# Performance work log

Hardware: AMD Instinct MI355X
Metric: run time of the kernel (lower is better)

## Reference

```python
import jax, jax.numpy as jnp
import numpy as np

D_MODEL = 1024
H = 4
DK = 128   # head_qk_dim (key_dim=512)
DV = 256   # head_v_dim (value_dim=1024)
EPS = 1e-5
SCALE = DK ** -0.5


def setup_inputs() -> dict:
    key = jax.random.key(0)
    ks = jax.random.split(key, 8)
    w = lambda k, i, o: jax.random.normal(k, (i, o), jnp.float32) * (2.0 ** -2.5) * (6.0 / (i + o)) ** 0.5 * 2
    return {
        "x": jax.random.normal(ks[0], (2, 4096, D_MODEL), jnp.float32),
        "Wq": w(ks[1], D_MODEL, H * DK),
        "Wk": w(ks[2], D_MODEL, H * DK),
        "Wv": w(ks[3], D_MODEL, H * DV),
        "Wb": w(ks[4], D_MODEL, H),
        "Wg": w(ks[5], D_MODEL, H * DV),
        "Wo": w(ks[6], H * DV, D_MODEL),
        "norm_w": jnp.ones((DV,), jnp.float32),
    }


def _delta_rule(q, k, v, beta):
    """Delta-rule linear attention. q,k: [b,n,h,dk], v: [b,n,h,dv], beta: [b,n,h].
    S_t = S_{t-1} + k_t (beta_t * (v_t - k_t^T S_{t-1}))^T ; o_t = q_t^T S_t."""
    b = q.shape[0]
    # time-major for scan: [n,b,h,*]
    qt = jnp.moveaxis(q, 1, 0)
    kt = jnp.moveaxis(k, 1, 0)
    vt = jnp.moveaxis(v, 1, 0)
    bt = jnp.moveaxis(beta, 1, 0)
    S0 = jnp.zeros((b, H, DK, DV), q.dtype)

    def step(S, inp):
        q_t, k_t, v_t, b_t = inp
        pred = jnp.einsum('bhk,bhkv->bhv', k_t, S)          # current memory readout
        delta = (v_t - pred) * b_t[..., None]                # beta-scaled error
        S = S + k_t[..., :, None] * delta[..., None, :]      # rank-1 update [b,h,dk,dv]
        o_t = jnp.einsum('bhk,bhkv->bhv', q_t, S)
        return S, o_t

    _, o = jax.lax.scan(step, S0, (qt, kt, vt, bt))          # o: [n,b,h,dv]
    return jnp.moveaxis(o, 0, 1)                             # [b,n,h,dv]


def reference(x, Wq, Wk, Wv, Wb, Wg, Wo, norm_w):
    b, n, _ = x.shape
    q = (x @ Wq).reshape(b, n, H, DK)
    k = (x @ Wk).reshape(b, n, H, DK)
    v = (x @ Wv).reshape(b, n, H, DV)
    beta = jax.nn.sigmoid(x @ Wb)                            # [b,n,h]
    # L2-normalize keys (delta-rule kernels assume unit-norm k) and scale q
    k = k * jax.lax.rsqrt(jnp.sum(k * k, axis=-1, keepdims=True) + 1e-12)
    q = q * SCALE
    o = _delta_rule(q, k, v, beta)                           # [b,n,h,dv]
    # FusedRMSNormSwishGate over head_v_dim
    g = (x @ Wg).reshape(b, n, H, DV)
    o = o * jax.lax.rsqrt(jnp.mean(o * o, axis=-1, keepdims=True) + EPS) * norm_w
    o = o * (g * jax.nn.sigmoid(g))                          # swish gate
    return o.reshape(b, n, H * DV) @ Wo
```

## Files before the change

### kernel.cpp

```cpp
#include <hip/hip_runtime.h>
#include <hip/hip_bf16.h>
#include <stdint.h>
#include <stddef.h>

typedef __attribute__((ext_vector_type(8))) short short8v;
typedef __attribute__((ext_vector_type(4))) float f32x4;
typedef unsigned short us;

__device__ __forceinline__ float bf2f(unsigned short u) {
    return __uint_as_float(((unsigned int)u) << 16);
}
__device__ __forceinline__ unsigned short f2bf(float f) {
    unsigned int x = __float_as_uint(f);
    x += 0x7fffu + ((x >> 16) & 1u);
    return (unsigned short)(x >> 16);
}
__device__ __forceinline__ unsigned int cvtpk(float lo, float hi) {
    unsigned int r;
    asm("v_cvt_pk_bf16_f32 %0, %1, %2" : "=v"(r) : "v"(lo), "v"(hi));
    return r;
}

#define NTOK 8192
#define DM   1024
#define NPROJ 3072
#define SEQ  4096
#define NCHUNK 64
#define SCQ 0.08838834764831845f

#define GLDS16(g, l) __builtin_amdgcn_global_load_lds( \
    (const __attribute__((address_space(1))) void*)(g), \
    (__attribute__((address_space(3))) void*)(l), 16, 0, 0)

__device__ __forceinline__ void bar_lgkm() {
    asm volatile("s_waitcnt lgkmcnt(0)" ::: "memory");
    __builtin_amdgcn_s_barrier();
    __builtin_amdgcn_sched_barrier(0);
}

__device__ __forceinline__ int sw16(int row, int k) {
    int u = k >> 3;
    int us_ = (u & 8) | ((u ^ row) & 7);
    return row * 128 + us_ * 8 + (k & 7);
}
__device__ __forceinline__ int sw8(int row, int k) {
    int u = k >> 3;
    int us_ = (u ^ row) & 7;
    return row * 64 + us_ * 8 + (k & 7);
}
__device__ __forceinline__ int sw128(int row, int k) {
    int u = k >> 3;
    return row * 128 + ((u ^ row) & 15) * 8 + (k & 7);
}
__device__ __forceinline__ int sw64(int row, int k) {
    int u = k >> 3;
    return row * 64 + ((u ^ row) & 7) * 8 + (k & 7);
}
__device__ __forceinline__ int sw64b(int row, int k) {
    int u = k >> 3;
    return row * 64 + ((u ^ row ^ (row >> 3)) & 7) * 8 + (k & 7);
}
__device__ __forceinline__ int swU(int t, int j) {
    int jj = j & 127, u = jj >> 3;
    int us_ = (u & 8) | ((u ^ t) & 7);
    return t * 256 + (j >> 7) * 128 + us_ * 8 + (jj & 7);
}
__device__ __forceinline__ int swU128(int t, int jj) {
    int u = jj >> 3;
    int us_ = (u & 8) | ((u ^ t) & 7);
    return t * 128 + us_ * 8 + (jj & 7);
}

__global__ void convert_x(const float* __restrict__ x, us* __restrict__ xb, int nunits) {
    int i = blockIdx.x * 256 + threadIdx.x;
    if (i >= nunits) return;
    int tok = i >> 7;
    int kb = (i >> 3) & 15;
    int u = i & 7;
    int ko = kb * 64 + ((u ^ (tok & 7)) * 8);
    const float4* src = (const float4*)(x + (size_t)tok * 1024 + ko);
    float4 v0 = src[0], v1 = src[1];
    uint4 o;
    o.x = cvtpk(v0.x, v0.y); o.y = cvtpk(v0.z, v0.w);
    o.z = cvtpk(v1.x, v1.y); o.w = cvtpk(v1.z, v1.w);
    *(uint4*)(xb + (size_t)i * 8) = o;
}

__global__ __launch_bounds__(256) void transpose_w(const float* __restrict__ src,
                                                   us* __restrict__ dst, int K, int N) {
    __shared__ float tl[64][65];
    int k0 = blockIdx.y * 64, n0 = blockIdx.x * 64;
    int tid = threadIdx.x;
    int tr = tid >> 6, tc = tid & 63;
    #pragma unroll
    for (int i = 0; i < 16; i++) {
        int kk = 4 * i + tr;
        tl[kk][tc] = src[(size_t)(k0 + kk) * N + n0 + tc];
    }
    __syncthreads();
    int n = tid >> 2, seg = (tid & 3) * 16;
    short8v a, b;
    #pragma unroll
    for (int e = 0; e < 8; e++) {
        a[e] = (short)f2bf(tl[seg + e][n]);
        b[e] = (short)f2bf(tl[seg + 8 + e][n]);
    }
    int n_ = n0 + n;
    int o1 = (tid & 3) * 2, o2_ = o1 + 1;
    us* d = dst + (size_t)n_ * K + k0;
    *(short8v*)(d + (o1 ^ (n_ & 7)) * 8) = a;
    *(short8v*)(d + (o2_ ^ (n_ & 7)) * 8) = b;
}

__global__ __launch_bounds__(256) void beta_kernel(const float* __restrict__ x,
                                                   const float* __restrict__ Wb,
                                                   float* __restrict__ beta) {
    __shared__ float part[16][16][4];
    int tl = threadIdx.x >> 4, sg = threadIdx.x & 15;
    int tok = blockIdx.x * 16 + tl;
    const float4* xr = (const float4*)(x + (size_t)tok * DM);
    const float4* wb = (const float4*)Wb;
    float s0 = 0.f, s1 = 0.f, s2 = 0.f, s3 = 0.f;
    #pragma unroll
    for (int it = 0; it < 16; it++) {
        int f = it * 16 + sg;
        float4 xv = xr[f];
        float4 w0 = wb[4 * f + 0], w1 = wb[4 * f + 1], w2 = wb[4 * f + 2], w3 = wb[4 * f + 3];
        s0 += xv.x * w0.x + xv.y * w1.x + xv.z * w2.x + xv.w * w3.x;
        s1 += xv.x * w0.y + xv.y * w1.y + xv.z * w2.y + xv.w * w3.y;
        s2 += xv.x * w0.z + xv.y * w1.z + xv.z * w2.z + xv.w * w3.z;
        s3 += xv.x * w0.w + xv.y * w1.w + xv.z * w2.w + xv.w * w3.w;
    }
    part[tl][sg][0] = s0; part[tl][sg][1] = s1; part[tl][sg][2] = s2; part[tl][sg][3] = s3;
    __syncthreads();
    if (threadIdx.x < 64) {
        int tl2 = threadIdx.x >> 2, h = threadIdx.x & 3;
        float s = 0.f;
        #pragma unroll
        for (int g = 0; g < 16; g++) s += part[tl2][g][h];
        beta[(size_t)(blockIdx.x * 16 + tl2) * 4 + h] = 1.f / (1.f + __expf(-s));
    }
}

template<int OUT_F32>
__global__ __launch_bounds__(256) void gemm_bt(
    const us* __restrict__ A, const us* __restrict__ BT,
    void* __restrict__ C, int M, int N, int K)
{
    __shared__ us As[128][64];
    __shared__ us Bs[128][64];
    int tid = threadIdx.x;
    int wave = tid >> 6, lane = tid & 63;
    int wr = (wave >> 1) * 64, wc = (wave & 1) * 64;
    int fr = lane & 15, fq = lane >> 4;
    int nbx = gridDim.x, nwg = nbx * gridDim.y;
    int wg = blockIdx.y * nbx + blockIdx.x;
    int cpx = nwg >> 3;
    wg = (wg & 7) * cpx + (wg >> 3);
    int m0 = (wg % nbx) * 128, n0 = (wg / nbx) * 128;

    f32x4 acc[4][4];
    #pragma unroll
    for (int i = 0; i < 4; i++)
        #pragma unroll
        for (int j = 0; j < 4; j++) acc[i][j] = (f32x4){0.f, 0.f, 0.f, 0.f};

    int rl = lane >> 3, ul = lane & 7;

    for (int k0 = 0; k0 < K; k0 += 64) {
        #pragma unroll
        for (int i = 0; i < 4; i++) {
            int row = wave * 32 + i * 8 + rl;
            GLDS16(&A[(size_t)(m0 + row) * K + k0 + ul * 8], &As[0][0] + (wave * 32 + i * 8) * 64);
            GLDS16(&BT[(size_t)(n0 + row) * K + k0 + ul * 8], &Bs[0][0] + (wave * 32 + i * 8) * 64);
        }
        __syncthreads();
        #pragma unroll
        for (int kk = 0; kk < 2; kk++) {
            short8v a[4], b[4];
            #pragma unroll
            for (int i = 0; i < 4; i++) {
                int ra = wr + i * 16 + fr;
                a[i] = *(const short8v*)&As[ra][((4 * kk + fq) ^ (ra & 7)) * 8];
                int rb = wc + i * 16 + fr;
                b[i] = *(const short8v*)&Bs[rb][((4 * kk + fq) ^ (rb & 7)) * 8];
            }
            #pragma unroll
            for (int i = 0; i < 4; i++)
                #pragma unroll
                for (int j = 0; j < 4; j++)
                    acc[i][j] = __builtin_amdgcn_mfma_f32_16x16x32_bf16(a[i], b[j], acc[i][j], 0, 0, 0);
        }
        __syncthreads();
    }
    #pragma unroll
    for (int i = 0; i < 4; i++)
        #pragma unroll
        for (int j = 0; j < 4; j++)
            #pragma unroll
            for (int t = 0; t < 4; t++) {
                int row = m0 + wr + i * 16 + fq * 4 + t;
                int col = n0 + wc + j * 16 + fr;
                float val = acc[i][j][t];
                if (OUT_F32) ((float*)C)[(size_t)row * N + col] = val;
                else ((us*)C)[(size_t)row * N + col] = f2bf(val);
            }
}

__global__ __launch_bounds__(256) void chunk_pre(
    const us* __restrict__ QKVG, const float* __restrict__ beta,
    us* __restrict__ Wbuf, us* __restrict__ Ubuf,
    us* __restrict__ Pbuf, us* __restrict__ KTbuf)
{
    __shared__ us Ks[8192];
    __shared__ us KTs[8192];
    __shared__ us VT[8192];
    __shared__ us Tb[4096];
    __shared__ float Af[64][64];
    __shared__ float betas[64];

    int c = blockIdx.x, bh = blockIdx.y;
    int b = bh >> 2, h = bh & 3;
    int tid = threadIdx.x;
    int wv = tid >> 6, ln = tid & 63;
    int fr = ln & 15, fq = ln >> 4;
    int tok0 = b * SEQ + c * 64;
    size_t cb = (size_t)bh * NCHUNK + c;

    #pragma unroll
    for (int r = 0; r < 4; r++) {
        int idx = tid + 256 * r;
        int t = idx >> 4, u = idx & 15;
        short8v kv = *(const short8v*)(QKVG + (size_t)(tok0 + t) * NPROJ + 512 + h * 128 + u * 8);
        *(short8v*)(Ks + sw16(t, u * 8)) = kv;
    }
    if (tid < 64) betas[tid] = beta[(size_t)(tok0 + tid) * 4 + h];
    __syncthreads();

    {
        int t = tid >> 2, p = tid & 3;
        short8v v[4];
        float ss = 0.f;
        #pragma unroll
        for (int uu = 0; uu < 4; uu++) {
            v[uu] = *(const short8v*)(Ks + sw16(t, (p * 4 + uu) * 8));
            #pragma unroll
            for (int e = 0; e < 8; e++) {
                float f = bf2f((unsigned short)v[uu][e]);
                ss += f * f;
            }
        }
        ss += __shfl_xor(ss, 1);
        ss += __shfl_xor(ss, 2);
        float rn = rsqrtf(ss + 1e-12f);
        #pragma unroll
        for (int uu = 0; uu < 4; uu++) {
            short8v o;
            #pragma unroll
            for (int e = 0; e < 8; e++)
                o[e] = (short)f2bf(bf2f((unsigned short)v[uu][e]) * rn);
            *(short8v*)(Ks + sw16(t, (p * 4 + uu) * 8)) = o;
        }
    }
    __syncthreads();

    {
        f32x4 aacc[4];
        #pragma unroll
        for (int jt = 0; jt < 4; jt++) aacc[jt] = (f32x4){0.f, 0.f, 0.f, 0.f};
        #pragma unroll
        for (int ks = 0; ks < 4; ks++) {
            short8v ak = *(const short8v*)(Ks + sw16(16 * wv + fr, 32 * ks + 8 * fq));
            #pragma unroll
            for (int jt = 0; jt < 4; jt++) {
                short8v bk = *(const short8v*)(Ks + sw16(16 * jt + fr, 32 * ks + 8 * fq));
                aacc[jt] = __builtin_amdgcn_mfma_f32_16x16x32_bf16(ak, bk, aacc[jt], 0, 0, 0);
            }
        }
        #pragma unroll
        for (int jt = 0; jt < 4; jt++)
            #pragma unroll
            for (int r = 0; r < 4; r++) {
                int t = 16 * wv + 4 * fq + r, s = 16 * jt + fr;
                if (s < t) Af[t][s] = betas[t] * aacc[jt][r];
            }
    }
    __syncthreads();

    if (wv == 0) {
        int cc = ln;
        for (int tb = 0; tb < 8; tb++) {
            int base = tb * 8;
            float xs[8];
            #pragma unroll
            for (int i = 0; i < 8; i++) {
                int t = base + i;
                float v = Af[t][cc];
                #pragma unroll
                for (int s = 0; s < i; s++)
                    v += Af[t][base + s] * xs[s];
                float xt = (cc < t) ? -v : 0.f;
                xs[i] = xt;
                if (cc < t) Af[t][cc] = xt;
            }
            for (int r = base + 8; r < 64; r += 2) {
                float u0 = 0.f, u1 = 0.f;
                #pragma unroll
                for (int s = 0; s < 8; s++) {
                    float a0 = Af[r][base + s];
                    float a1 = Af[r + 1][base + s];
                    u0 += a0 * xs[s];
                    u1 += a1 * xs[s];
                }
                Af[r][cc] += u0;
                Af[r + 1][cc] += u1;
            }
        }
    } else {
        int q = tid - 64;
        for (int g = q; g < 1024; g += 192) {
            int t = g >> 4, u = g & 15;
            short8v kv = *(const short8v*)(Ks + sw16(t, u * 8));
            #pragma unroll
            for (int e = 0; e < 8; e++)
                KTs[sw64b(u * 8 + e, t)] = (unsigned short)kv[e];
        }
        for (int g = q; g < 1024; g += 192) {
            int t = g >> 4, jg = g & 15;
            short8v vv = *(const short8v*)(QKVG + (size_t)(tok0 + t) * NPROJ + 1024 + h * 256 + jg * 8);
            #pragma unroll
            for (int e = 0; e < 8; e++)
                VT[sw64b(jg * 8 + e, t)] = (unsigned short)vv[e];
        }
    }
    __syncthreads();

    {
        f32x4 pacc[4];
        #pragma unroll
        for (int jt = 0; jt < 4; jt++) pacc[jt] = (f32x4){0.f, 0.f, 0.f, 0.f};
        #pragma unroll
        for (int ks = 0; ks < 4; ks++) {
            short8v aq = *(const short8v*)(QKVG + (size_t)(tok0 + 16 * wv + fr) * NPROJ + h * 128 + ks * 32 + fq * 8);
            #pragma unroll
            for (int jt = 0; jt < 4; jt++) {
                short8v bk = *(const short8v*)(Ks + sw16(16 * jt + fr, 32 * ks + 8 * fq));
                pacc[jt] = __builtin_amdgcn_mfma_f32_16x16x32_bf16(aq, bk, pacc[jt], 0, 0, 0);
            }
        }
        #pragma unroll
        for (int jt = 0; jt < 4; jt++)
            #pragma unroll
            for (int r = 0; r < 4; r++) {
                int t = 16 * wv + 4 * fq + r, s = 16 * jt + fr;
                float val = (s <= t) ? pacc[jt][r] * SCQ : 0.f;
                Pbuf[cb * 4096 + sw64(t, s)] = f2bf(val);
            }
        #pragma unroll
        for (int i = 0; i < 16; i++) {
            int idx = tid + 256 * i;
            int t = idx >> 6, s = idx & 63;
            float tv = (s < t) ? Af[t][s] : (s == t ? 1.f : 0.f);
            Tb[sw8(t, s)] = f2bf(tv * betas[s]);
        }
        #pragma unroll
        for (int i = 0; i < 4; i++) {
            int idx = tid + 256 * i;
            *(short8v*)(KTbuf + cb * 8192 + (size_t)idx * 8) =
                *(const short8v*)(KTs + (size_t)idx * 8);
        }
    }
    __syncthreads();

    {
        f32x4 wacc[8], uacc[8];
        #pragma unroll
        for (int jt = 0; jt < 8; jt++) {
            wacc[jt] = (f32x4){0.f, 0.f, 0.f, 0.f};
            uacc[jt] = (f32x4){0.f, 0.f, 0.f, 0.f};
        }
        #pragma unroll
        for (int ks = 0; ks < 2; ks++) {
            short8v at = *(const short8v*)(Tb + sw8(16 * wv + fr, 32 * ks + 8 * fq));
            #pragma unroll
            for (int jt = 0; jt < 8; jt++) {
                short8v bk = *(const short8v*)(KTs + sw64b(16 * jt + fr, 32 * ks + 8 * fq));
                wacc[jt] = __builtin_amdgcn_mfma_f32_16x16x32_bf16(at, bk, wacc[jt], 0, 0, 0);
                short8v bv = *(const short8v*)(VT + sw64b(16 * jt + fr, 32 * ks + 8 * fq));
                uacc[jt] = __builtin_amdgcn_mfma_f32_16x16x32_bf16(at, bv, uacc[jt], 0, 0, 0);
            }
        }
        #pragma unroll
        for (int jt = 0; jt < 8; jt++)
            #pragma unroll
            for (int r = 0; r < 4; r++) {
                int t = 16 * wv + 4 * fq + r, d = 16 * jt + fr;
                Wbuf[cb * 8192 + (d >> 6) * 4096 + sw64(t, d & 63)] = f2bf(-wacc[jt][r]);
                Ubuf[cb * 16384 + swU(t, d)] = f2bf(uacc[jt][r]);
            }
    }
    __syncthreads();

    #pragma unroll
    for (int i = 0; i < 4; i++) {
        int g = tid + 256 * i;
        int t = g >> 4, jg = g & 15;
        short8v vv = *(const short8v*)(QKVG + (size_t)(tok0 + t) * NPROJ + 1024 + h * 256 + 128 + jg * 8);
        #pragma unroll
        for (int e = 0; e < 8; e++)
            VT[sw64b(jg * 8 + e, t)] = (unsigned short)vv[e];
    }
    __syncthreads();
    {
        f32x4 uacc[8];
        #pragma unroll
        for (int jt = 0; jt < 8; jt++) uacc[jt] = (f32x4){0.f, 0.f, 0.f, 0.f};
        #pragma unroll
        for (int ks = 0; ks < 2; ks++) {
            short8v at = *(const short8v*)(Tb + sw8(16 * wv + fr, 32 * ks + 8 * fq));
            #pragma unroll
            for (int jt = 0; jt < 8; jt++) {
                short8v bv = *(const short8v*)(VT + sw64b(16 * jt + fr, 32 * ks + 8 * fq));
                uacc[jt] = __builtin_amdgcn_mfma_f32_16x16x32_bf16(at, bv, uacc[jt], 0, 0, 0);
            }
        }
        #pragma unroll
        for (int jt = 0; jt < 8; jt++)
            #pragma unroll
            for (int r = 0; r < 4; r++) {
                int t = 16 * wv + 4 * fq + r, j = 16 * jt + fr;
                Ubuf[cb * 16384 + swU(t, 128 + j)] = f2bf(uacc[jt][r]);
            }
    }
}

#define SCW 0
#define SCKT 8192
#define SCU 16384
#define SCBUF 17408
#define SSTB (2 * SCBUF)
#define SDTB (2 * SCBUF + 2048)

__global__ __launch_bounds__(128, 1) void scan_mfma(
    const us* __restrict__ Wbuf, const us* __restrict__ Ubuf,
    const us* __restrict__ KTbuf, us* __restrict__ Sbuf)
{
    extern __shared__ us lds[];
    int tid = threadIdx.x;
    int wv = tid >> 6, ln = tid & 63;
    int fr = ln & 15, fq = ln >> 4;
    int sl = blockIdx.x >> 3;
    int j0 = sl * 16;
    int bh = blockIdx.x & 7;

    short8v id0;
    #pragma unroll
    for (int e = 0; e < 8; e++)
        id0[e] = (short)((8 * fq + e == fr) ? 0x3F80 : 0);

    f32x4 sacc[4];
    #pragma unroll
    for (int i = 0; i < 4; i++) sacc[i] = (f32x4){0.f, 0.f, 0.f, 0.f};

    us* ST = lds + SSTB + wv * 1024;

    auto issue = [&](int c1) {
        size_t cb = (size_t)bh * NCHUNK + c1;
        us* dst = lds + (c1 & 1) * SCBUF;
        const us* Wc = Wbuf + cb * 8192 + wv * 4096;
        const us* Kc = KTbuf + cb * 8192 + wv * 4096;
        #pragma unroll
        for (int i = 0; i < 8; i++) {
            GLDS16(Wc + i * 512 + ln * 8, dst + SCW + wv * 4096 + i * 512);
            GLDS16(Kc + i * 512 + ln * 8, dst + SCKT + wv * 4096 + i * 512);
        }
        if (wv) {
            const us* Uc = Ubuf + cb * 16384;
            #pragma unroll
            for (int i = 0; i < 2; i++) {
                int t = i * 32 + (ln >> 1);
                GLDS16(Uc + swU(t, j0 + (ln & 1) * 8), dst + SCU + i * 512);
            }
        }
    };

    issue(0);

    for (int c = 0; c < NCHUNK; c++) {
        const us* ba = lds + (c & 1) * SCBUF;
        us* DTw = lds + SDTB + (c & 1) * 2048 + wv * 1024;
        const us* DTr = lds + SDTB + (c & 1) * 2048;
        size_t sb = ((size_t)bh * NCHUNK + c) * 32768 + sl * 2048 + wv * 1024;

        #pragma unroll
        for (int dt = 0; dt < 4; dt++) {
            uint2 w;
            w.x = cvtpk(sacc[dt][0], sacc[dt][1]);
            w.y = cvtpk(sacc[dt][2], sacc[dt][3]);
            int dl = 16 * dt + 4 * fq;
            int off = fr * 64 + (((dl >> 3) ^ fr) & 7) * 8 + (dl & 7);
            *(uint2*)&ST[off] = w;
            *(uint2*)(Sbuf + sb + off) = w;
        }
        if (c + 1 < NCHUNK) issue(c + 1);
        if (c + 1 < NCHUNK) {
            if (wv) asm volatile("s_waitcnt vmcnt(22)" ::: "memory");
            else    asm volatile("s_waitcnt vmcnt(20)" ::: "memory");
        } else {
            asm volatile("s_waitcnt vmcnt(4)" ::: "memory");
        }
        __builtin_amdgcn_sched_barrier(0);

        f32x4 dacc[4];
        #pragma unroll
        for (int tt = 0; tt < 4; tt++) dacc[tt] = (f32x4){0.f, 0.f, 0.f, 0.f};
        #pragma unroll
        for (int kc = 0; kc < 2; kc++) {
            short8v bs = *(const short8v*)&ST[fr * 64 + (((4 * kc + fq) ^ fr) & 7) * 8];
            #pragma unroll
            for (int tt = 0; tt < 4; tt++) {
                short8v aw = *(const short8v*)&ba[SCW + wv * 4096 + sw64(16 * tt + fr, 32 * kc + 8 * fq)];
                dacc[tt] = __builtin_amdgcn_mfma_f32_16x16x32_bf16(aw, bs, dacc[tt], 0, 0, 0);
            }
        }
        if (wv) {
            #pragma unroll
            for (int tt = 0; tt < 4; tt++) {
                short8v au = *(const short8v*)&ba[SCU + (16 * tt + fr) * 16 + 8 * (fq & 1)];
                dacc[tt] = __builtin_amdgcn_mfma_f32_16x16x32_bf16(au, id0, dacc[tt], 0, 0, 0);
            }
        }
        #pragma unroll
        for (int tt = 0; tt < 4; tt++) {
            uint2 w;
            w.x = cvtpk(dacc[tt][0], dacc[tt][1]);
            w.y = cvtpk(dacc[tt][2], dacc[tt][3]);
            int tl = 16 * tt + 4 * fq;
            *(uint2*)&DTw[fr * 64 + (((tl >> 3) ^ fr) & 7) * 8 + (tl & 7)] = w;
        }
        bar_lgkm();
        #pragma unroll
        for (int kc2 = 0; kc2 < 2; kc2++) {
            int o = fr * 64 + (((4 * kc2 + fq) ^ fr) & 7) * 8;
            short8v bd0 = *(const short8v*)&DTr[o];
            short8v bd1 = *(const short8v*)&DTr[1024 + o];
            #pragma unroll
            for (int dt = 0; dt < 4; dt++) {
                short8v ak = *(const short8v*)&ba[SCKT + sw64b(64 * wv + 16 * dt + fr, 32 * kc2 + 8 * fq)];
                sacc[dt] = __builtin_amdgcn_mfma_f32_16x16x32_bf16(ak, bd0, sacc[dt], 0, 0, 0);
                sacc[dt] = __builtin_amdgcn_mfma_f32_16x16x32_bf16(ak, bd1, sacc[dt], 0, 0, 0);
            }
        }
    }
}

#define K2_W 0
#define K2_P 8192
#define K2_U 12288
#define K2_S 20480
#define K2_Q 36864
#define K2_DT 45056

__global__ __launch_bounds__(256, 1) void out_k(
    const us* __restrict__ QKVG, const us* __restrict__ Wbuf,
    const us* __restrict__ Ubuf, const us* __restrict__ Pbuf,
    const us* __restrict__ Sbuf, us* __restrict__ Ob)
{
    extern __shared__ us lds[];
    int tid = threadIdx.x;
    int wv = tid >> 6, ln = tid & 63;
    int fr = ln & 15, fq = ln >> 4;
    int c = blockIdx.x;
    int bh = blockIdx.y >> 1, jh = blockIdx.y & 1;
    int b = bh >> 2, h = bh & 3;
    int tok0 = b * SEQ + c * 64;
    size_t cb = (size_t)bh * NCHUNK + c;

    short8v id0, id1;
    #pragma unroll
    for (int e = 0; e < 8; e++) {
        id0[e] = (short)((8 * fq + e == fr) ? 0x3F80 : 0);
        id1[e] = (short)((8 * fq + e == fr + 16) ? 0x3F80 : 0);
    }

    #pragma unroll
    for (int i = 0; i < 4; i++) {
        int q = (i * 4 + wv) * 512 + ln * 8;
        GLDS16(Wbuf + cb * 8192 + q, lds + K2_W + (i * 4 + wv) * 512);
    }
    #pragma unroll
    for (int i = 0; i < 2; i++) {
        int q = (i * 4 + wv) * 512 + ln * 8;
        GLDS16(Pbuf + cb * 4096 + q, lds + K2_P + (i * 4 + wv) * 512);
    }
    #pragma unroll
    for (int i = 0; i < 4; i++) {
        int q = (i * 4 + wv) * 512 + ln * 8;
        int t = q >> 7, r = q & 127;
        GLDS16(Ubuf + cb * 16384 + t * 256 + jh * 128 + r, lds + K2_U + (i * 4 + wv) * 512);
    }
    size_t sbase = cb * 32768 + (size_t)jh * 16384;
    #pragma unroll
    for (int i = 0; i < 8; i++) {
        int q = (i * 4 + wv) * 512 + ln * 8;
        GLDS16(Sbuf + sbase + q, lds + K2_S + (i * 4 + wv) * 512);
    }
    short8v qv[4];
    #pragma unroll
    for (int i = 0; i < 4; i++) {
        int idx = tid + 256 * i;
        int t = idx >> 4, u = idx & 15;
        qv[i] = *(const short8v*)(QKVG + (size_t)(tok0 + t) * NPROJ + h * 128 + u * 8);
    }
    #pragma unroll
    for (int i = 0; i < 4; i++) {
        int idx = tid + 256 * i;
        int t = idx >> 4, u = idx & 15;
        *(short8v*)&lds[K2_Q + sw128(t, u * 8)] = qv[i];
    }
    __syncthreads();

    f32x4 dacc[8], oacc[8];
    #pragma unroll
    for (int jt = 0; jt < 8; jt++) {
        dacc[jt] = (f32x4){0.f, 0.f, 0.f, 0.f};
        oacc[jt] = (f32x4){0.f, 0.f, 0.f, 0.f};
    }
    #pragma unroll
    for (int ks = 0; ks < 4; ks++) {
        short8v aw = *(const short8v*)&lds[K2_W + (ks >> 1) * 4096
            + sw64(16 * wv + fr, (ks & 1) * 32 + 8 * fq)];
        short8v aq = *(const short8v*)&lds[K2_Q + sw128(16 * wv + fr, 32 * ks + 8 * fq)];
        #pragma unroll
        for (int jt = 0; jt < 8; jt++) {
            short8v bs = *(const short8v*)&lds[K2_S + jt * 2048 + (ks >> 1) * 1024
                + fr * 64 + ((((ks & 1) * 4 + fq) ^ fr) & 7) * 8];
            dacc[jt] = __builtin_amdgcn_mfma_f32_16x16x32_bf16(aw, bs, dacc[jt], 0, 0, 0);
            oacc[jt] = __builtin_amdgcn_mfma_f32_16x16x32_bf16(aq, bs, oacc[jt], 0, 0, 0);
        }
    }
    #pragma unroll
    for (int ju = 0; ju < 4; ju++) {
        short8v au = *(const short8v*)&lds[K2_U + swU128(16 * wv + fr, 32 * ju + 8 * fq)];
        dacc[2 * ju + 0] = __builtin_amdgcn_mfma_f32_16x16x32_bf16(au, id0, dacc[2 * ju + 0], 0, 0, 0);
        dacc[2 * ju + 1] = __builtin_amdgcn_mfma_f32_16x16x32_bf16(au, id1, dacc[2 * ju + 1], 0, 0, 0);
    }
    #pragma unroll
    for (int jt = 0; jt < 8; jt++)
        #pragma unroll
        for (int r = 0; r < 4; r++) oacc[jt][r] *= SCQ;
    #pragma unroll
    for (int jt = 0; jt < 8; jt++) {
        int j = 16 * jt + fr;
        int t0 = 16 * wv + 4 * fq;
        uint2 w;
        w.x = cvtpk(dacc[jt][0], dacc[jt][1]);
        w.y = cvtpk(dacc[jt][2], dacc[jt][3]);
        *(uint2*)&lds[K2_DT + sw64(j, t0)] = w;
    }
    bar_lgkm();

    #pragma unroll
    for (int ks = 0; ks < 2; ks++) {
        short8v ap = *(const short8v*)&lds[K2_P + sw64(16 * wv + fr, 32 * ks + 8 * fq)];
        #pragma unroll
        for (int jt = 0; jt < 8; jt++) {
            short8v bd = *(const short8v*)&lds[K2_DT + sw64(16 * jt + fr, 32 * ks + 8 * fq)];
            oacc[jt] = __builtin_amdgcn_mfma_f32_16x16x32_bf16(ap, bd, oacc[jt], 0, 0, 0);
        }
    }
    us* ob = Ob + (size_t)tok0 * 1024 + h * 256 + jh * 128;
    #pragma unroll
    for (int jt = 0; jt < 8; jt++)
        #pragma unroll
        for (int r = 0; r < 4; r++) {
            int t = 16 * wv + 4 * fq + r;
            ob[(size_t)t * 1024 + 16 * jt + fr] = f2bf(oacc[jt][r]);
        }
}

__global__ __launch_bounds__(256) void gate_norm(const us* __restrict__ Ob,
                                                 const us* __restrict__ QKVG,
                                                 const float* __restrict__ norm_w,
                                                 us* __restrict__ o2)
{
    int gid = blockIdx.x * 4 + (threadIdx.x >> 6);
    int ln = threadIdx.x & 63;
    int tok = gid >> 2, h = gid & 3;
    size_t base = (size_t)tok * 1024 + h * 256 + ln * 4;
    uint2 ov = *(const uint2*)&Ob[base];
    float o0 = bf2f((us)ov.x), o1 = bf2f((us)(ov.x >> 16));
    float o2v = bf2f((us)ov.y), o3 = bf2f((us)(ov.y >> 16));
    float ss = o0 * o0 + o1 * o1 + o2v * o2v + o3 * o3;
    #pragma unroll
    for (int off = 32; off; off >>= 1) ss += __shfl_xor(ss, off);
    float r = rsqrtf(ss * (1.0f / 256.0f) + 1e-5f);
    uint2 gv = *(const uint2*)&QKVG[(size_t)tok * NPROJ + 2048 + h * 256 + ln * 4];
    float g0 = bf2f((us)gv.x), g1 = bf2f((us)(gv.x >> 16));
    float g2 = bf2f((us)gv.y), g3 = bf2f((us)(gv.y >> 16));
    float4 nw = *(const float4*)&norm_w[ln * 4];
    float r0 = o0 * r * nw.x * (g0 / (1.f + __expf(-g0)));
    float r1 = o1 * r * nw.y * (g1 / (1.f + __expf(-g1)));
    float r2 = o2v * r * nw.z * (g2 / (1.f + __expf(-g2)));
    float r3 = o3 * r * nw.w * (g3 / (1.f + __expf(-g3)));
    uint2 w;
    w.x = cvtpk(r0, r1);
    w.y = cvtpk(r2, r3);
    int u = h * 32 + (ln >> 1);
    size_t dsto = (size_t)tok * 1024 + (size_t)(u >> 3) * 64
                + (size_t)(((u & 7) ^ (tok & 7)) * 8) + (ln & 1) * 4;
    *(uint2*)&o2[dsto] = w;
}

extern "C" void kernel_launch(void* const* d_in, const int* in_sizes, int n_in,
                              void* d_out, int out_size, void* d_ws, size_t ws_size,
                              hipStream_t stream) {
    const float* x      = (const float*)d_in[0];
    const float* Wq     = (const float*)d_in[1];
    const float* Wk     = (const float*)d_in[2];
    const float* Wv     = (const float*)d_in[3];
    const float* Wb     = (const float*)d_in[4];
    const float* Wg     = (const float*)d_in[5];
    const float* Wo     = (const float*)d_in[6];
    const float* norm_w = (const float*)d_in[7];
    float* out = (float*)d_out;

    char* ws = (char*)d_ws;
    us*    xb   = (us*)(ws + 0);
    us*    WT   = (us*)(ws + 16777216);
    us*    Sbuf = (us*)(ws + 0);
    us*    KTbuf= (us*)(ws + 33554432);
    us*    Ob   = (us*)(ws + 33554432);
    us*    QKVG = (us*)(ws + 50331648);
    float* beta = (float*)(ws + 100663296);
    us*    Wbuf = (us*)(ws + 100794368);
    us*    Ubuf = (us*)(ws + 109182976);
    us*    o2   = (us*)(ws + 109182976);
    us*    Pbuf = (us*)(ws + 125960192);
    us*    WoT  = (us*)(ws + 130154496);

    (void)hipFuncSetAttribute((const void*)scan_mfma,
                              hipFuncAttributeMaxDynamicSharedMemorySize, 81920);
    (void)hipFuncSetAttribute((const void*)out_k,
                              hipFuncAttributeMaxDynamicSharedMemorySize, 106496);

    convert_x<<<NTOK * 128 / 256, 256, 0, stream>>>(x, xb, NTOK * 128);
    transpose_w<<<dim3(8, 16), 256, 0, stream>>>(Wq, WT, DM, 512);
    transpose_w<<<dim3(8, 16), 256, 0, stream>>>(Wk, WT + (size_t)512 * DM, DM, 512);
    transpose_w<<<dim3(16, 16), 256, 0, stream>>>(Wv, WT + (size_t)1024 * DM, DM, 1024);
    transpose_w<<<dim3(16, 16), 256, 0, stream>>>(Wg, WT + (size_t)2048 * DM, DM, 1024);
    transpose_w<<<dim3(16, 16), 256, 0, stream>>>(Wo, WoT, DM, 1024);
    beta_kernel<<<NTOK / 16, 256, 0, stream>>>(x, Wb, beta);
    gemm_bt<0><<<dim3(64, 24), 256, 0, stream>>>(xb, WT, (void*)QKVG, NTOK, NPROJ, DM);
    chunk_pre<<<dim3(NCHUNK, 8), 256, 0, stream>>>(QKVG, beta, Wbuf, Ubuf, Pbuf, KTbuf);
    scan_mfma<<<128, 128, 81920, stream>>>(Wbuf, Ubuf, KTbuf, Sbuf);
    out_k<<<dim3(NCHUNK, 16), 256, 106496, stream>>>(QKVG, Wbuf, Ubuf, Pbuf, Sbuf, Ob);
    gate_norm<<<NTOK, 256, 0, stream>>>(Ob, QKVG, norm_w, o2);
    gemm_bt<1><<<dim3(64, 8), 256, 0, stream>>>(o2, WoT, (void*)out, NTOK, DM, DM);
}
```

Before: 274.1 us.

## Overlap Q and G projection GEMM with sequential scan in a fused kernel

The first projection GEMM now computes only the K and V columns. The Q and G projection tiles run as extra workgroups inside the scan kernel, so they fill CUs left idle by the 128 latency-bound scan blocks. The causal QK^T intra-chunk score matrix moves from chunk_pre into out_k, which now loads a swizzled K copy instead of a precomputed P buffer. The workspace layout is reshuffled to fit the changes. The risks are contention between the GEMM blocks and the scan blocks for memory bandwidth, and idle half-blocks in the scan part.

```diff
diff --git a/kernel.cpp b/kernel.cpp
--- a/kernel.cpp
+++ b/kernel.cpp
@@ -210,7 +210,7 @@
 __global__ __launch_bounds__(256) void chunk_pre(
     const us* __restrict__ QKVG, const float* __restrict__ beta,
     us* __restrict__ Wbuf, us* __restrict__ Ubuf,
-    us* __restrict__ Pbuf, us* __restrict__ KTbuf)
+    us* __restrict__ Kbuf, us* __restrict__ KTbuf)
 {
     __shared__ us Ks[8192];
     __shared__ us KTs[8192];
@@ -336,26 +336,13 @@
     __syncthreads();
 
     {
-        f32x4 pacc[4];
-        #pragma unroll
-        for (int jt = 0; jt < 4; jt++) pacc[jt] = (f32x4){0.f, 0.f, 0.f, 0.f};
-        #pragma unroll
-        for (int ks = 0; ks < 4; ks++) {
-            short8v aq = *(const short8v*)(QKVG + (size_t)(tok0 + 16 * wv + fr) * NPROJ + h * 128 + ks * 32 + fq * 8);
-            #pragma unroll
-            for (int jt = 0; jt < 4; jt++) {
-                short8v bk = *(const short8v*)(Ks + sw16(16 * jt + fr, 32 * ks + 8 * fq));
-                pacc[jt] = __builtin_amdgcn_mfma_f32_16x16x32_bf16(aq, bk, pacc[jt], 0, 0, 0);
-            }
-        }
-        #pragma unroll
-        for (int jt = 0; jt < 4; jt++)
-            #pragma unroll
-            for (int r = 0; r < 4; r++) {
-                int t = 16 * wv + 4 * fq + r, s = 16 * jt + fr;
-                float val = (s <= t) ? pacc[jt][r] * SCQ : 0.f;
-                Pbuf[cb * 4096 + sw64(t, s)] = f2bf(val);
-            }
+        #pragma unroll
+        for (int i = 0; i < 4; i++) {
+            int idx = tid + 256 * i;
+            int t = idx >> 4, u = idx & 15;
+            short8v kv = *(const short8v*)(Ks + sw16(t, u * 8));
+            *(short8v*)(Kbuf + cb * 8192 + t * 128 + (size_t)(((u ^ t) & 15) * 8)) = kv;
+        }
         #pragma unroll
         for (int i = 0; i < 16; i++) {
             int idx = tid + 256 * i;
@@ -441,116 +428,183 @@
 #define SSTB (2 * SCBUF)
 #define SDTB (2 * SCBUF + 2048)
 
-__global__ __launch_bounds__(128, 1) void scan_mfma(
+__global__ __launch_bounds__(256, 1) void fused_scan_qg(
+    const us* __restrict__ xb, const us* __restrict__ WT, us* __restrict__ QKVG,
     const us* __restrict__ Wbuf, const us* __restrict__ Ubuf,
     const us* __restrict__ KTbuf, us* __restrict__ Sbuf)
 {
     extern __shared__ us lds[];
     int tid = threadIdx.x;
-    int wv = tid >> 6, ln = tid & 63;
-    int fr = ln & 15, fq = ln >> 4;
-    int sl = blockIdx.x >> 3;
-    int j0 = sl * 16;
-    int bh = blockIdx.x & 7;
-
-    short8v id0;
-    #pragma unroll
-    for (int e = 0; e < 8; e++)
-        id0[e] = (short)((8 * fq + e == fr) ? 0x3F80 : 0);
-
-    f32x4 sacc[4];
-    #pragma unroll
-    for (int i = 0; i < 4; i++) sacc[i] = (f32x4){0.f, 0.f, 0.f, 0.f};
-
-    us* ST = lds + SSTB + wv * 1024;
-
-    auto issue = [&](int c1) {
-        size_t cb = (size_t)bh * NCHUNK + c1;
-        us* dst = lds + (c1 & 1) * SCBUF;
-        const us* Wc = Wbuf + cb * 8192 + wv * 4096;
-        const us* Kc = KTbuf + cb * 8192 + wv * 4096;
-        #pragma unroll
-        for (int i = 0; i < 8; i++) {
-            GLDS16(Wc + i * 512 + ln * 8, dst + SCW + wv * 4096 + i * 512);
-            GLDS16(Kc + i * 512 + ln * 8, dst + SCKT + wv * 4096 + i * 512);
-        }
-        if (wv) {
-            const us* Uc = Ubuf + cb * 16384;
-            #pragma unroll
-            for (int i = 0; i < 2; i++) {
-                int t = i * 32 + (ln >> 1);
-                GLDS16(Uc + swU(t, j0 + (ln & 1) * 8), dst + SCU + i * 512);
-            }
-        }
-    };
-
-    issue(0);
-
-    for (int c = 0; c < NCHUNK; c++) {
-        const us* ba = lds + (c & 1) * SCBUF;
-        us* DTw = lds + SDTB + (c & 1) * 2048 + wv * 1024;
-        const us* DTr = lds + SDTB + (c & 1) * 2048;
-        size_t sb = ((size_t)bh * NCHUNK + c) * 32768 + sl * 2048 + wv * 1024;
-
-        #pragma unroll
-        for (int dt = 0; dt < 4; dt++) {
-            uint2 w;
-            w.x = cvtpk(sacc[dt][0], sacc[dt][1]);
-            w.y = cvtpk(sacc[dt][2], sacc[dt][3]);
-            int dl = 16 * dt + 4 * fq;
-            int off = fr * 64 + (((dl >> 3) ^ fr) & 7) * 8 + (dl & 7);
-            *(uint2*)&ST[off] = w;
-            *(uint2*)(Sbuf + sb + off) = w;
-        }
-        if (c + 1 < NCHUNK) issue(c + 1);
-        if (c + 1 < NCHUNK) {
-            if (wv) asm volatile("s_waitcnt vmcnt(22)" ::: "memory");
-            else    asm volatile("s_waitcnt vmcnt(20)" ::: "memory");
-        } else {
-            asm volatile("s_waitcnt vmcnt(4)" ::: "memory");
-        }
-        __builtin_amdgcn_sched_barrier(0);
-
-        f32x4 dacc[4];
-        #pragma unroll
-        for (int tt = 0; tt < 4; tt++) dacc[tt] = (f32x4){0.f, 0.f, 0.f, 0.f};
-        #pragma unroll
-        for (int kc = 0; kc < 2; kc++) {
-            short8v bs = *(const short8v*)&ST[fr * 64 + (((4 * kc + fq) ^ fr) & 7) * 8];
+
+    if (blockIdx.x < 128) {
+        if (tid >= 128) {
+            for (int c = 0; c < NCHUNK; c++) __builtin_amdgcn_s_barrier();
+            return;
+        }
+        int wv = tid >> 6, ln = tid & 63;
+        int fr = ln & 15, fq = ln >> 4;
+        int sl = blockIdx.x >> 3;
+        int j0 = sl * 16;
+        int bh = blockIdx.x & 7;
+
+        short8v id0;
+        #pragma unroll
+        for (int e = 0; e < 8; e++)
+            id0[e] = (short)((8 * fq + e == fr) ? 0x3F80 : 0);
+
+        f32x4 sacc[4];
+        #pragma unroll
+        for (int i = 0; i < 4; i++) sacc[i] = (f32x4){0.f, 0.f, 0.f, 0.f};
+
+        us* ST = lds + SSTB + wv * 1024;
+
+        auto issue = [&](int c1) {
+            size_t cb = (size_t)bh * NCHUNK + c1;
+            us* dst = lds + (c1 & 1) * SCBUF;
+            const us* Wc = Wbuf + cb * 8192 + wv * 4096;
+            const us* Kc = KTbuf + cb * 8192 + wv * 4096;
+            #pragma unroll
+            for (int i = 0; i < 8; i++) {
+                GLDS16(Wc + i * 512 + ln * 8, dst + SCW + wv * 4096 + i * 512);
+                GLDS16(Kc + i * 512 + ln * 8, dst + SCKT + wv * 4096 + i * 512);
+            }
+            if (wv) {
+                const us* Uc = Ubuf + cb * 16384;
+                #pragma unroll
+                for (int i = 0; i < 2; i++) {
+                    int t = i * 32 + (ln >> 1);
+                    GLDS16(Uc + swU(t, j0 + (ln & 1) * 8), dst + SCU + i * 512);
+                }
+            }
+        };
+
+        issue(0);
+
+        for (int c = 0; c < NCHUNK; c++) {
+            const us* ba = lds + (c & 1) * SCBUF;
+            us* DTw = lds + SDTB + (c & 1) * 2048 + wv * 1024;
+            const us* DTr = lds + SDTB + (c & 1) * 2048;
+            size_t sb = ((size_t)bh * NCHUNK + c) * 32768 + sl * 2048 + wv * 1024;
+
+            #pragma unroll
+            for (int dt = 0; dt < 4; dt++) {
+                uint2 w;
+                w.x = cvtpk(sacc[dt][0], sacc[dt][1]);
+                w.y = cvtpk(sacc[dt][2], sacc[dt][3]);
+                int dl = 16 * dt + 4 * fq;
+                int off = fr * 64 + (((dl >> 3) ^ fr) & 7) * 8 + (dl & 7);
+                *(uint2*)&ST[off] = w;
+                *(uint2*)(Sbuf + sb + off) = w;
+            }
+            if (c + 1 < NCHUNK) issue(c + 1);
+            if (c + 1 < NCHUNK) {
+                if (wv) asm volatile("s_waitcnt vmcnt(22)" ::: "memory");
+                else    asm volatile("s_waitcnt vmcnt(20)" ::: "memory");
+            } else {
+                asm volatile("s_waitcnt vmcnt(4)" ::: "memory");
+            }
+            __builtin_amdgcn_sched_barrier(0);
+
+            f32x4 dacc[4];
+            #pragma unroll
+            for (int tt = 0; tt < 4; tt++) dacc[tt] = (f32x4){0.f, 0.f, 0.f, 0.f};
+            #pragma unroll
+            for (int kc = 0; kc < 2; kc++) {
+                short8v bs = *(const short8v*)&ST[fr * 64 + (((4 * kc + fq) ^ fr) & 7) * 8];
+                #pragma unroll
+                for (int tt = 0; tt < 4; tt++) {
+                    short8v aw = *(const short8v*)&ba[SCW + wv * 4096 + sw64(16 * tt + fr, 32 * kc + 8 * fq)];
+                    dacc[tt] = __builtin_amdgcn_mfma_f32_16x16x32_bf16(aw, bs, dacc[tt], 0, 0, 0);
+                }
+            }
+            if (wv) {
+                #pragma unroll
+                for (int tt = 0; tt < 4; tt++) {
+                    short8v au = *(const short8v*)&ba[SCU + (16 * tt + fr) * 16 + 8 * (fq & 1)];
+                    dacc[tt] = __builtin_amdgcn_mfma_f32_16x16x32_bf16(au, id0, dacc[tt], 0, 0, 0);
+                }
+            }
             #pragma unroll
             for (int tt = 0; tt < 4; tt++) {
-                short8v aw = *(const short8v*)&ba[SCW + wv * 4096 + sw64(16 * tt + fr, 32 * kc + 8 * fq)];
-                dacc[tt] = __builtin_amdgcn_mfma_f32_16x16x32_bf16(aw, bs, dacc[tt], 0, 0, 0);
-            }
-        }
-        if (wv) {
-            #pragma unroll
-            for (int tt = 0; tt < 4; tt++) {
-                short8v au = *(const short8v*)&ba[SCU + (16 * tt + fr) * 16 + 8 * (fq & 1)];
-                dacc[tt] = __builtin_amdgcn_mfma_f32_16x16x32_bf16(au, id0, dacc[tt], 0, 0, 0);
-            }
-        }
-        #pragma unroll
-        for (int tt = 0; tt < 4; tt++) {
-            uint2 w;
-            w.x = cvtpk(dacc[tt][0], dacc[tt][1]);
-            w.y = cvtpk(dacc[tt][2], dacc[tt][3]);
-            int tl = 16 * tt + 4 * fq;
-            *(uint2*)&DTw[fr * 64 + (((tl >> 3) ^ fr) & 7) * 8 + (tl & 7)] = w;
-        }
-        bar_lgkm();
-        #pragma unroll
-        for (int kc2 = 0; kc2 < 2; kc2++) {
-            int o = fr * 64 + (((4 * kc2 + fq) ^ fr) & 7) * 8;
-            short8v bd0 = *(const short8v*)&DTr[o];
-            short8v bd1 = *(const short8v*)&DTr[1024 + o];
-            #pragma unroll
-            for (int dt = 0; dt < 4; dt++) {
-                short8v ak = *(const short8v*)&ba[SCKT + sw64b(64 * wv + 16 * dt + fr, 32 * kc2 + 8 * fq)];
-                sacc[dt] = __builtin_amdgcn_mfma_f32_16x16x32_bf16(ak, bd0, sacc[dt], 0, 0, 0);
-                sacc[dt] = __builtin_amdgcn_mfma_f32_16x16x32_bf16(ak, bd1, sacc[dt], 0, 0, 0);
-            }
-        }
+                uint2 w;
+                w.x = cvtpk(dacc[tt][0], dacc[tt][1]);
+                w.y = cvtpk(dacc[tt][2], dacc[tt][3]);
+                int tl = 16 * tt + 4 * fq;
+                *(uint2*)&DTw[fr * 64 + (((tl >> 3) ^ fr) & 7) * 8 + (tl & 7)] = w;
+            }
+            bar_lgkm();
+            #pragma unroll
+            for (int kc2 = 0; kc2 < 2; kc2++) {
+                int o = fr * 64 + (((4 * kc2 + fq) ^ fr) & 7) * 8;
+                short8v bd0 = *(const short8v*)&DTr[o];
+                short8v bd1 = *(const short8v*)&DTr[1024 + o];
+                #pragma unroll
+                for (int dt = 0; dt < 4; dt++) {
+                    short8v ak = *(const short8v*)&ba[SCKT + sw64b(64 * wv + 16 * dt + fr, 32 * kc2 + 8 * fq)];
+                    sacc[dt] = __builtin_amdgcn_mfma_f32_16x16x32_bf16(ak, bd0, sacc[dt], 0, 0, 0);
+                    sacc[dt] = __builtin_amdgcn_mfma_f32_16x16x32_bf16(ak, bd1, sacc[dt], 0, 0, 0);
+                }
+            }
+        }
+        return;
+    }
+
+    {
+        us* As = lds;
+        us* Bs = lds + 8192;
+        int wave = tid >> 6, lane = tid & 63;
+        int wr = (wave >> 1) * 64, wc = (wave & 1) * 64;
+        int fr = lane & 15, fq = lane >> 4;
+        int wg = blockIdx.x - 128;
+        wg = (wg & 7) * 96 + (wg >> 3);
+        int m0 = (wg % 64) * 128;
+        int ntile = wg / 64;
+        int n0 = ntile * 128 + (ntile >= 4 ? 1536 : 0);
+
+        f32x4 acc[4][4];
+        #pragma unroll
+        for (int i = 0; i < 4; i++)
+            #pragma unroll
+            for (int j = 0; j < 4; j++) acc[i][j] = (f32x4){0.f, 0.f, 0.f, 0.f};
+
+        int rl = lane >> 3, ul = lane & 7;
+
+        for (int k0 = 0; k0 < DM; k0 += 64) {
+            #pragma unroll
+            for (int i = 0; i < 4; i++) {
+                int row = wave * 32 + i * 8 + rl;
+                GLDS16(&xb[(size_t)(m0 + row) * DM + k0 + ul * 8], As + (wave * 32 + i * 8) * 64);
+                GLDS16(&WT[(size_t)(n0 + row) * DM + k0 + ul * 8], Bs + (wave * 32 + i * 8) * 64);
+            }
+            __syncthreads();
+            #pragma unroll
+            for (int kk = 0; kk < 2; kk++) {
+                short8v a[4], b[4];
+                #pragma unroll
+                for (int i = 0; i < 4; i++) {
+                    int ra = wr + i * 16 + fr;
+                    a[i] = *(const short8v*)&As[ra * 64 + ((4 * kk + fq) ^ (ra & 7)) * 8];
+                    int rb = wc + i * 16 + fr;
+                    b[i] = *(const short8v*)&Bs[rb * 64 + ((4 * kk + fq) ^ (rb & 7)) * 8];
+                }
+                #pragma unroll
+                for (int i = 0; i < 4; i++)
+                    #pragma unroll
+                    for (int j = 0; j < 4; j++)
+                        acc[i][j] = __builtin_amdgcn_mfma_f32_16x16x32_bf16(a[i], b[j], acc[i][j], 0, 0, 0);
+            }
+            __syncthreads();
+        }
+        #pragma unroll
+        for (int i = 0; i < 4; i++)
+            #pragma unroll
+            for (int j = 0; j < 4; j++)
+                #pragma unroll
+                for (int t = 0; t < 4; t++) {
+                    int row = m0 + wr + i * 16 + fq * 4 + t;
+                    int col = n0 + wc + j * 16 + fr;
+                    QKVG[(size_t)row * NPROJ + col] = f2bf(acc[i][j][t]);
+                }
     }
 }
 
@@ -560,10 +614,11 @@
 #define K2_S 20480
 #define K2_Q 36864
 #define K2_DT 45056
+#define K2_K 49152
 
 __global__ __launch_bounds__(256, 1) void out_k(
     const us* __restrict__ QKVG, const us* __restrict__ Wbuf,
-    const us* __restrict__ Ubuf, const us* __restrict__ Pbuf,
+    const us* __restrict__ Ubuf, const us* __restrict__ Kbuf,
     const us* __restrict__ Sbuf, us* __restrict__ Ob)
 {
     extern __shared__ us lds[];
@@ -589,9 +644,9 @@
         GLDS16(Wbuf + cb * 8192 + q, lds + K2_W + (i * 4 + wv) * 512);
     }
     #pragma unroll
-    for (int i = 0; i < 2; i++) {
+    for (int i = 0; i < 4; i++) {
         int q = (i * 4 + wv) * 512 + ln * 8;
-        GLDS16(Pbuf + cb * 4096 + q, lds + K2_P + (i * 4 + wv) * 512);
+        GLDS16(Kbuf + cb * 8192 + q, lds + K2_K + (i * 4 + wv) * 512);
     }
     #pragma unroll
     for (int i = 0; i < 4; i++) {
@@ -644,6 +699,28 @@
         short8v au = *(const short8v*)&lds[K2_U + swU128(16 * wv + fr, 32 * ju + 8 * fq)];
         dacc[2 * ju + 0] = __builtin_amdgcn_mfma_f32_16x16x32_bf16(au, id0, dacc[2 * ju + 0], 0, 0, 0);
         dacc[2 * ju + 1] = __builtin_amdgcn_mfma_f32_16x16x32_bf16(au, id1, dacc[2 * ju + 1], 0, 0, 0);
+    }
+    {
+        f32x4 pacc[4];
+        #pragma unroll
+        for (int jt2 = 0; jt2 < 4; jt2++) pacc[jt2] = (f32x4){0.f, 0.f, 0.f, 0.f};
+        #pragma unroll
+        for (int ks = 0; ks < 4; ks++) {
+            short8v aq = *(const short8v*)&lds[K2_Q + sw128(16 * wv + fr, 32 * ks + 8 * fq)];
+            #pragma unroll
+            for (int jt2 = 0; jt2 < 4; jt2++) {
+                short8v bk = *(const short8v*)&lds[K2_K + sw128(16 * jt2 + fr, 32 * ks + 8 * fq)];
+                pacc[jt2] = __builtin_amdgcn_mfma_f32_16x16x32_bf16(aq, bk, pacc[jt2], 0, 0, 0);
+            }
+        }
+        #pragma unroll
+        for (int jt2 = 0; jt2 < 4; jt2++)
+            #pragma unroll
+            for (int r = 0; r < 4; r++) {
+                int t = 16 * wv + 4 * fq + r, s = 16 * jt2 + fr;
+                float val = (s <= t) ? pacc[jt2][r] * SCQ : 0.f;
+                lds[K2_P + sw64(t, s)] = f2bf(val);
+            }
     }
     #pragma unroll
     for (int jt = 0; jt < 8; jt++)
@@ -727,22 +804,22 @@
 
     char* ws = (char*)d_ws;
     us*    xb   = (us*)(ws + 0);
+    us*    Ob   = (us*)(ws + 0);
     us*    WT   = (us*)(ws + 16777216);
-    us*    Sbuf = (us*)(ws + 0);
-    us*    KTbuf= (us*)(ws + 33554432);
-    us*    Ob   = (us*)(ws + 33554432);
-    us*    QKVG = (us*)(ws + 50331648);
-    float* beta = (float*)(ws + 100663296);
-    us*    Wbuf = (us*)(ws + 100794368);
-    us*    Ubuf = (us*)(ws + 109182976);
-    us*    o2   = (us*)(ws + 109182976);
-    us*    Pbuf = (us*)(ws + 125960192);
-    us*    WoT  = (us*)(ws + 130154496);
-
-    (void)hipFuncSetAttribute((const void*)scan_mfma,
+    us*    KTbuf= (us*)(ws + 23068672);
+    us*    QKVG = (us*)(ws + 31457280);
+    float* beta = (float*)(ws + 81788928);
+    us*    Wbuf = (us*)(ws + 81920000);
+    us*    Ubuf = (us*)(ws + 90308608);
+    us*    o2   = (us*)(ws + 90308608);
+    us*    Kbuf = (us*)(ws + 107085824);
+    us*    WoT  = (us*)(ws + 115474432);
+    us*    Sbuf = (us*)(ws + 117571584);
+
+    (void)hipFuncSetAttribute((const void*)fused_scan_qg,
                               hipFuncAttributeMaxDynamicSharedMemorySize, 81920);
     (void)hipFuncSetAttribute((const void*)out_k,
-                              hipFuncAttributeMaxDynamicSharedMemorySize, 106496);
+                              hipFuncAttributeMaxDynamicSharedMemorySize, 114688);
 
     convert_x<<<NTOK * 128 / 256, 256, 0, stream>>>(x, xb, NTOK * 128);
     transpose_w<<<dim3(8, 16), 256, 0, stream>>>(Wq, WT, DM, 512);
@@ -751,10 +828,11 @@
     transpose_w<<<dim3(16, 16), 256, 0, stream>>>(Wg, WT + (size_t)2048 * DM, DM, 1024);
     transpose_w<<<dim3(16, 16), 256, 0, stream>>>(Wo, WoT, DM, 1024);
     beta_kernel<<<NTOK / 16, 256, 0, stream>>>(x, Wb, beta);
-    gemm_bt<0><<<dim3(64, 24), 256, 0, stream>>>(xb, WT, (void*)QKVG, NTOK, NPROJ, DM);
-    chunk_pre<<<dim3(NCHUNK, 8), 256, 0, stream>>>(QKVG, beta, Wbuf, Ubuf, Pbuf, KTbuf);
-    scan_mfma<<<128, 128, 81920, stream>>>(Wbuf, Ubuf, KTbuf, Sbuf);
-    out_k<<<dim3(NCHUNK, 16), 256, 106496, stream>>>(QKVG, Wbuf, Ubuf, Pbuf, Sbuf, Ob);
+    gemm_bt<0><<<dim3(64, 12), 256, 0, stream>>>(xb, WT + (size_t)512 * DM,
+                                                 (void*)(QKVG + 512), NTOK, NPROJ, DM);
+    chunk_pre<<<dim3(NCHUNK, 8), 256, 0, stream>>>(QKVG, beta, Wbuf, Ubuf, Kbuf, KTbuf);
+    fused_scan_qg<<<896, 256, 81920, stream>>>(xb, WT, QKVG, Wbuf, Ubuf, KTbuf, Sbuf);
+    out_k<<<dim3(NCHUNK, 16), 256, 114688, stream>>>(QKVG, Wbuf, Ubuf, Kbuf, Sbuf, Ob);
     gate_norm<<<NTOK, 256, 0, stream>>>(Ob, QKVG, norm_w, o2);
     gemm_bt<1><<<dim3(64, 8), 256, 0, stream>>>(o2, WoT, (void*)out, NTOK, DM, DM);
 }
```

Result: faster. 247.4 us (-9.8%).
